# Performance work log

Measured on AMD Instinct MI355X. Metric: run time of the kernel, lower is better.

## Reference

```python
import jax, jax.numpy as jnp
import numpy as np

B, S, D, H, M, E, K = 4, 2048, 1024, 2048, 64, 8, 2  # batch, seq, d_model, max_neurons, moe_hidden, experts, top_k


def setup_inputs() -> dict:
    key = jax.random.key(0)
    ks = jax.random.split(key, 10)
    r = lambda k, shape: jax.random.normal(k, shape, dtype=jnp.float32) * 0.02
    return {
        "inputs_embeds": jax.random.normal(ks[0], (B, S, D), dtype=jnp.float32),
        "enc_W": r(ks[1], (D, H)), "enc_b": jnp.zeros((H,), jnp.float32),
        "s2c_W": r(ks[2], (H, M)), "s2c_b": jnp.zeros((M,), jnp.float32),
        "rW1": r(ks[3], (M, 64)), "rb1": jnp.zeros((64,), jnp.float32),
        "rW2": r(ks[4], (64, E)), "rb2": jnp.zeros((E,), jnp.float32),
        "We1": r(ks[5], (E, M, H // 2)), "be1": jnp.zeros((E, H // 2), jnp.float32),
        "We2": r(ks[6], (E, H // 2, M)), "be2": jnp.zeros((E, M), jnp.float32),
        "c2s_W": r(ks[7], (M, H)), "c2s_b": jnp.zeros((H,), jnp.float32),
        "dec_W": r(ks[8], (H, D)), "dec_b": jnp.zeros((D,), jnp.float32),
        "ln_g": jnp.ones((D,), jnp.float32), "ln_b": jnp.zeros((D,), jnp.float32),
    }


def _layernorm(x, g, b, eps=1e-5):
    mu = x.mean(-1, keepdims=True)
    var = ((x - mu) ** 2).mean(-1, keepdims=True)
    return (x - mu) * jax.lax.rsqrt(var + eps) * g + b


def _forward(inputs_embeds, enc_W, enc_b, s2c_W, s2c_b, rW1, rb1, rW2, rb2,
             We1, be1, We2, be2, c2s_W, c2s_b, dec_W, dec_b, ln_g, ln_b):
    b, s, _ = inputs_embeds.shape
    # GIFNeuron encoder (rate-coded surrogate spikes)
    spikes_enc = jax.nn.sigmoid(inputs_embeds @ enc_W + enc_b)          # (B,S,H)
    flat = spikes_enc.reshape(b * s, H)                                  # (N,H)
    # SpikeToContinuousBridge ('rate'): projection to MoE hidden
    cont = flat @ s2c_W + s2c_b                                          # (N,M)
    # LiquidMoERouter: 2-layer router, softmax, top-k, renormalize
    logits = jnp.tanh(cont @ rW1 + rb1) @ rW2 + rb2                      # (N,E)
    probs = jax.nn.softmax(logits, axis=-1)
    topw, topi = jax.lax.top_k(probs, K)                                 # (N,K)
    w = topw / topw.sum(-1, keepdims=True)
    # dense per-token per-expert gate == sum_k weights[:,k] * (indices[:,k]==e)
    gates = (jax.nn.one_hot(topi, E, dtype=cont.dtype) * w[..., None]).sum(1)  # (N,E)
    # SNNExpert MLP per expert, dense dispatch + weighted combine (index_add equivalent)
    h = jax.nn.relu(jnp.einsum('nm,emh->enh', cont, We1) + be1[:, None, :])    # (E,N,H/2)
    expert_out = jnp.einsum('enh,ehm->enm', h, We2) + be2[:, None, :]          # (E,N,M)
    output_flat = jnp.einsum('enm,ne->nm', expert_out, gates)                  # (N,M)
    # ContinuousToSpikeBridge ('poisson', expected rate), 2D -> 1 timestep
    spikes_moe = jax.nn.sigmoid(output_flat @ c2s_W + c2s_b).reshape(b, s, H)
    # GIFNeuron decoder + LayerNorm
    decoded = jax.nn.sigmoid(spikes_moe @ dec_W + dec_b)                 # (B,S,D)
    return _layernorm(decoded, ln_g, ln_b)


def reference(inputs_embeds, enc_W, enc_b, s2c_W, s2c_b, rW1, rb1, rW2, rb2,
              We1, be1, We2, be2, c2s_W, c2s_b, dec_W, dec_b, ln_g, ln_b):
    return _forward(inputs_embeds, enc_W, enc_b, s2c_W, s2c_b, rW1, rb1, rW2, rb2,
                    We1, be1, We2, be2, c2s_W, c2s_b, dec_W, dec_b, ln_g, ln_b)
```

## Files before the change

kernel.cpp:

```cpp
#include <hip/hip_runtime.h>
#include <hip/hip_bf16.h>
#include <cstdint>
#include <cstddef>

#define TOK    8192
#define DMODEL 1024
#define HDIM   2048
#define MDIM   64
#define NEXP   8
#define HHALF  1024

using f32x4  = __attribute__((ext_vector_type(4))) float;
using bf16x8 = __attribute__((ext_vector_type(8))) __bf16;
using bf16x4 = __attribute__((ext_vector_type(4))) __bf16;

__device__ __forceinline__ void async16(const void* g, void* l) {
  __builtin_amdgcn_global_load_lds(
      (const __attribute__((address_space(1))) unsigned int*)g,
      (__attribute__((address_space(3))) unsigned int*)l, 16, 0, 0);
}

__global__ __launch_bounds__(256) void preamble_kernel(
    const float* __restrict__ X, __bf16* __restrict__ Xb,
    const float* __restrict__ encW, __bf16* __restrict__ encWT,
    const float* __restrict__ s2cW, __bf16* __restrict__ s2cWT,
    const float* __restrict__ c2sW, __bf16* __restrict__ c2sWT,
    const float* __restrict__ decW, __bf16* __restrict__ decWT,
    const float* __restrict__ We1, __bf16* __restrict__ We1T,
    const float* __restrict__ We2, __bf16* __restrict__ We2T) {
  __shared__ float ts[32][33];
  const int tid = threadIdx.x;
  int b = blockIdx.x;
  if (b < 8192) {
    int i = b * 256 + tid;
    float4 v = ((const float4*)X)[i];
    bf16x4 o = { (__bf16)v.x, (__bf16)v.y, (__bf16)v.z, (__bf16)v.w };
    ((bf16x4*)Xb)[i] = o;
    return;
  }
  b -= 8192;
  const float* in; __bf16* outp; int R, C, tx, ty;
  if (b < 2048)              { in = encW; outp = encWT; R = 1024; C = 2048; tx = b % 64; ty = b / 64; }
  else if ((b -= 2048) < 128){ in = s2cW; outp = s2cWT; R = 2048; C = 64;   tx = b % 2;  ty = b / 2;  }
  else if ((b -= 128) < 128) { in = c2sW; outp = c2sWT; R = 64;   C = 2048; tx = b % 64; ty = b / 64; }
  else if ((b -= 128) < 2048){ in = decW; outp = decWT; R = 2048; C = 1024; tx = b % 32; ty = b / 32; }
  else if ((b -= 2048) < 512){ int s = b / 64, t = b % 64;
                               in = We1 + (size_t)s * 65536; outp = We1T + (size_t)s * 65536;
                               R = 64; C = 1024; tx = t % 32; ty = t / 32; }
  else                       { b -= 512; int s = b / 64, t = b % 64;
                               in = We2 + (size_t)s * 65536; outp = We2T + (size_t)s * 65536;
                               R = 1024; C = 64; tx = t % 2; ty = t / 2; }
  const int c0 = tx * 32, r0 = ty * 32;
  const int x = tid & 31, y = tid >> 5;
  #pragma unroll
  for (int i = y; i < 32; i += 8) ts[i][x] = in[(size_t)(r0 + i) * C + c0 + x];
  __syncthreads();
  #pragma unroll
  for (int i = y; i < 32; i += 8)
    outp[(size_t)(c0 + i) * R + r0 + x] = (__bf16)ts[x][i];
}
#define PREAMBLE_BLOCKS (8192 + 2048 + 128 + 128 + 2048 + 512 + 512)

template <int BN, int OUT_BF16, int ACT, int BIAS>
__global__ __launch_bounds__(512, 2) void gemm_8p(
    const __bf16* __restrict__ A, const __bf16* __restrict__ Bt,
    const float* __restrict__ bias, void* __restrict__ Cout,
    int M, int N, int K) {
  constexpr int BM = 256, BK = 64;
  constexpr int WTN = BN / 64;
  constexpr int A_LOADS = 4;
  constexpr int B_LOADS = BN / 64;
  __shared__ __bf16 As[2 * BM * BK];
  __shared__ __bf16 Bs[2 * BN * BK];
  const int tid = threadIdx.x;
  const int wave = tid >> 6, lane = tid & 63;
  const int quad = lane >> 4, l16 = lane & 15;
  const int m0 = blockIdx.x * BM, n0 = blockIdx.y * BN;
  const int wm = (wave & 1) * 128;
  const int wn = (wave >> 1) * (BN / 4);
  const int lrow = lane >> 3, lchunk = lane & 7;
  f32x4 acc[8][WTN] = {};

  const __bf16* aSrc[A_LOADS];
  const __bf16* bSrc[B_LOADS];
  #pragma unroll
  for (int t = 0; t < A_LOADS; ++t) {
    int row = (t * 8 + wave) * 8 + lrow;
    aSrc[t] = A + (size_t)(m0 + row) * K + (lchunk ^ (row & 7)) * 8;
  }
  #pragma unroll
  for (int t = 0; t < B_LOADS; ++t) {
    int row = (t * 8 + wave) * 8 + lrow;
    bSrc[t] = Bt + (size_t)(n0 + row) * K + (lchunk ^ (row & 7)) * 8;
  }
  int aOff[8], bOff[WTN];
  #pragma unroll
  for (int rf = 0; rf < 8; ++rf) {
    int row = wm + rf * 16 + l16;
    aOff[rf] = row * BK + ((quad ^ (row & 7)) * 8);
  }
  #pragma unroll
  for (int cf = 0; cf < WTN; ++cf) {
    int row = wn + cf * 16 + l16;
    bOff[cf] = row * BK + ((quad ^ (row & 7)) * 8);
  }

  auto stageA = [&](int t, __bf16* Ad) {
    async16(aSrc[t], Ad + (t * 8 + wave) * 8 * BK);
    aSrc[t] += BK;
  };
  auto stageB = [&](int t, __bf16* Bd) {
    async16(bSrc[t], Bd + (t * 8 + wave) * 8 * BK);
    bSrc[t] += BK;
  };

  __bf16 *curA = As, *nxtA = As + BM * BK;
  __bf16 *curB = Bs, *nxtB = Bs + BN * BK;
  const int nt = K / BK;

  stageB(0, curB); stageB(1, curB);
  if constexpr (BN == 256) { stageB(2, curB); stageB(3, curB); }
  stageA(0, curA); stageA(2, curA);
  stageA(1, curA); stageA(3, curA);
  asm volatile("s_waitcnt vmcnt(0)" ::: "memory");
  __builtin_amdgcn_s_barrier();

  for (int t = 0; t < nt; ++t) {
    const bool pre = (t + 1 < nt);
    bf16x8 af[4], bv[WTN];
    #pragma unroll
    for (int r = 0; r < 4; ++r) af[r] = *(const bf16x8*)(curA + aOff[r]);
    #pragma unroll
    for (int c = 0; c < WTN; ++c) bv[c] = *(const bf16x8*)(curB + bOff[c]);
    if (pre) {
      stageB(0, nxtB); stageB(1, nxtB);
      asm volatile("s_waitcnt vmcnt(2)" ::: "memory");
    } else {
      asm volatile("s_waitcnt vmcnt(0)" ::: "memory");
    }
    __builtin_amdgcn_s_barrier();
    __builtin_amdgcn_sched_barrier(0);
    __builtin_amdgcn_s_setprio(1);
    #pragma unroll
    for (int c = 0; c < WTN; ++c)
      #pragma unroll
      for (int r = 0; r < 4; ++r)
        acc[r][c] = __builtin_amdgcn_mfma_f32_16x16x32_bf16(af[r], bv[c], acc[r][c], 0, 0, 0);
    __builtin_amdgcn_s_setprio(0);
    __builtin_amdgcn_s_barrier();
    bf16x8 ag[4];
    #pragma unroll
    for (int r = 0; r < 4; ++r) ag[r] = *(const bf16x8*)(curA + aOff[4 + r]);
    if (pre) {
      if constexpr (BN == 256) { stageB(2, nxtB); stageB(3, nxtB); }
      else                     { stageA(0, nxtA); stageA(2, nxtA); }
    }
    __builtin_amdgcn_s_barrier();
    __builtin_amdgcn_sched_barrier(0);
    __builtin_amdgcn_s_setprio(1);
    #pragma unroll
    for (int c = 0; c < WTN; ++c)
      #pragma unroll
      for (int r = 0; r < 4; ++r)
        acc[4 + r][c] = __builtin_amdgcn_mfma_f32_16x16x32_bf16(ag[r], bv[c], acc[4 + r][c], 0, 0, 0);
    __builtin_amdgcn_s_setprio(0);
    __builtin_amdgcn_s_barrier();
    bf16x8 af2[4], bw[WTN];
    #pragma unroll
    for (int r = 0; r < 4; ++r) af2[r] = *(const bf16x8*)(curA + (aOff[r] ^ 32));
    #pragma unroll
    for (int c = 0; c < WTN; ++c) bw[c] = *(const bf16x8*)(curB + (bOff[c] ^ 32));
    if (pre) {
      if constexpr (BN == 256) { stageA(0, nxtA); stageA(2, nxtA); }
      else {
        stageA(1, nxtA); stageA(3, nxtA);
        asm volatile("s_waitcnt vmcnt(2)" ::: "memory");
      }
    }
    __builtin_amdgcn_s_barrier();
    __builtin_amdgcn_sched_barrier(0);
    __builtin_amdgcn_s_setprio(1);
    #pragma unroll
    for (int c = 0; c < WTN; ++c)
      #pragma unroll
      for (int r = 0; r < 4; ++r)
        acc[r][c] = __builtin_amdgcn_mfma_f32_16x16x32_bf16(af2[r], bw[c], acc[r][c], 0, 0, 0);
    __builtin_amdgcn_s_setprio(0);
    __builtin_amdgcn_s_barrier();
    bf16x8 ag2[4];
    #pragma unroll
    for (int r = 0; r < 4; ++r) ag2[r] = *(const bf16x8*)(curA + (aOff[4 + r] ^ 32));
    if (pre) {
      if constexpr (BN == 256) {
        stageA(1, nxtA); stageA(3, nxtA);
        asm volatile("s_waitcnt vmcnt(2)" ::: "memory");
      }
    }
    __builtin_amdgcn_s_barrier();
    __builtin_amdgcn_sched_barrier(0);
    __builtin_amdgcn_s_setprio(1);
    #pragma unroll
    for (int c = 0; c < WTN; ++c)
      #pragma unroll
      for (int r = 0; r < 4; ++r)
        acc[4 + r][c] = __builtin_amdgcn_mfma_f32_16x16x32_bf16(ag2[r], bw[c], acc[4 + r][c], 0, 0, 0);
    __builtin_amdgcn_s_setprio(0);
    __builtin_amdgcn_s_barrier();

    __bf16* x;
    x = curA; curA = nxtA; nxtA = x;
    x = curB; curB = nxtB; nxtB = x;
  }

  #pragma unroll
  for (int rf = 0; rf < 8; ++rf)
    #pragma unroll
    for (int cf = 0; cf < WTN; ++cf)
      #pragma unroll
      for (int r = 0; r < 4; ++r) {
        int m = m0 + wm + rf * 16 + quad * 4 + r;
        int n = n0 + wn + cf * 16 + l16;
        float v = acc[rf][cf][r];
        if (BIAS) v += bias[n];
        if (ACT == 1) v = 1.0f / (1.0f + __expf(-v));
        if (OUT_BF16)
          ((__bf16*)Cout)[(size_t)m * N + n] = (__bf16)v;
        else
          ((float*)Cout)[(size_t)m * N + n] = v;
      }
}

template <int BM, int BN, int WAVES, int OUT_BF16, int ACT, int BIAS, int SUMA>
__global__ __launch_bounds__(WAVES * 64) void gemm_bt(
    const __bf16* __restrict__ A, const __bf16* __restrict__ Bt,
    const float* __restrict__ bias, void* __restrict__ Cout,
    int M, int N, int K, const __bf16* __restrict__ A2) {
  constexpr int BK = 64;
  constexpr int WAVES_N = WAVES / 2;
  constexpr int WTM = BM / 32;
  constexpr int WTN = BN / (WAVES_N * 16);
  constexpr int NBUF = SUMA ? 1 : 2;
  constexpr int A_ISSUES = BM / (8 * WAVES);
  constexpr int B_ISSUES = BN / (8 * WAVES);
  __shared__ __bf16 As[NBUF * BM * BK];
  __shared__ __bf16 Bs[NBUF * BN * BK];
  const int tid = threadIdx.x;
  const int wave = tid >> 6, lane = tid & 63;
  const int quad = lane >> 4, l16 = lane & 15;
  const int m0 = blockIdx.x * BM, n0 = blockIdx.y * BN;
  const int ks = K / gridDim.z;
  const int kbeg = blockIdx.z * ks;
  const int wm = (wave & 1) * (BM / 2);
  const int wn = (wave >> 1) * (BN / WAVES_N);
  const int lrow = lane >> 3;
  const int lchunk = lane & 7;
  f32x4 acc[WTM][WTN] = {};

  const __bf16* aSrc[A_ISSUES];
  const __bf16* bSrc[B_ISSUES];
  #pragma unroll
  for (int t = 0; t < A_ISSUES; ++t) {
    int row = (t * WAVES + wave) * 8 + lrow;
    aSrc[t] = A + (size_t)(m0 + row) * K + kbeg + (lchunk ^ (row & 7)) * 8;
  }
  #pragma unroll
  for (int t = 0; t < B_ISSUES; ++t) {
    int row = (t * WAVES + wave) * 8 + lrow;
    bSrc[t] = Bt + (size_t)(n0 + row) * K + kbeg + (lchunk ^ (row & 7)) * 8;
  }
  int aOff[WTM][2], bOff[WTN][2];
  #pragma unroll
  for (int i = 0; i < WTM; ++i) {
    int row = wm + i * 16 + l16;
    #pragma unroll
    for (int kk = 0; kk < 2; ++kk)
      aOff[i][kk] = row * BK + (((kk * 4 + quad) ^ (row & 7)) * 8);
  }
  #pragma unroll
  for (int j = 0; j < WTN; ++j) {
    int row = wn + j * 16 + l16;
    #pragma unroll
    for (int kk = 0; kk < 2; ++kk)
      bOff[j][kk] = row * BK + (((kk * 4 + quad) ^ (row & 7)) * 8);
  }

  auto stage = [&](__bf16* Ad, __bf16* Bd) {
    #pragma unroll
    for (int t = 0; t < A_ISSUES; ++t) {
      async16(aSrc[t], Ad + (t * WAVES + wave) * 8 * BK);
      aSrc[t] += BK;
    }
    #pragma unroll
    for (int t = 0; t < B_ISSUES; ++t) {
      async16(bSrc[t], Bd + (t * WAVES + wave) * 8 * BK);
      bSrc[t] += BK;
    }
  };
  auto compute = [&](const __bf16* Ab, const __bf16* Bb) {
    #pragma unroll
    for (int kk = 0; kk < 2; ++kk) {
      bf16x8 af[WTM], bfr[WTN];
      #pragma unroll
      for (int i = 0; i < WTM; ++i) af[i] = *(const bf16x8*)(Ab + aOff[i][kk]);
      #pragma unroll
      for (int j = 0; j < WTN; ++j) bfr[j] = *(const bf16x8*)(Bb + bOff[j][kk]);
      #pragma unroll
      for (int i = 0; i < WTM; ++i)
        #pragma unroll
        for (int j = 0; j < WTN; ++j)
          acc[i][j] = __builtin_amdgcn_mfma_f32_16x16x32_bf16(af[i], bfr[j], acc[i][j], 0, 0, 0);
    }
  };

  const int niter = ks / BK;
  if constexpr (SUMA) {
    for (int it = 0; it < niter; ++it) {
      __syncthreads();
      #pragma unroll
      for (int t = 0; t < A_ISSUES; ++t) {
        int row = (t * WAVES + wave) * 8 + lrow;
        size_t go = (size_t)(m0 + row) * K + kbeg + it * BK + lchunk * 8;
        bf16x8 a0 = *(const bf16x8*)(A + go);
        bf16x8 a1 = *(const bf16x8*)(A2 + go);
        bf16x8 s;
        #pragma unroll
        for (int q = 0; q < 8; ++q) s[q] = (__bf16)((float)a0[q] + (float)a1[q]);
        *(bf16x8*)(As + row * BK + ((lchunk ^ (row & 7)) * 8)) = s;
      }
      #pragma unroll
      for (int t = 0; t < B_ISSUES; ++t) {
        async16(bSrc[t], Bs + (t * WAVES + wave) * 8 * BK);
        bSrc[t] += BK;
      }
      __syncthreads();
      compute(As, Bs);
    }
  } else {
    __bf16* curA = As;  __bf16* nxtA = As + BM * BK;
    __bf16* curB = Bs;  __bf16* nxtB = Bs + BN * BK;
    stage(curA, curB);
    asm volatile("s_waitcnt vmcnt(0)" ::: "memory");
    __builtin_amdgcn_s_barrier();
    for (int it = 0; it < niter - 1; ++it) {
      stage(nxtA, nxtB);
      compute(curA, curB);
      asm volatile("s_waitcnt vmcnt(0)" ::: "memory");
      __builtin_amdgcn_s_barrier();
      { __bf16* t = curA; curA = nxtA; nxtA = t; }
      { __bf16* t = curB; curB = nxtB; nxtB = t; }
    }
    compute(curA, curB);
  }

  char* Cz = (char*)Cout + (size_t)blockIdx.z * M * N * (OUT_BF16 ? 2 : 4);
  #pragma unroll
  for (int i = 0; i < WTM; ++i)
    #pragma unroll
    for (int j = 0; j < WTN; ++j)
      #pragma unroll
      for (int r = 0; r < 4; ++r) {
        int m = m0 + wm + i * 16 + quad * 4 + r;
        int n = n0 + wn + j * 16 + l16;
        float v = acc[i][j][r];
        if (BIAS) v += bias[n];
        if (ACT == 1) v = 1.0f / (1.0f + __expf(-v));
        if (OUT_BF16)
          ((__bf16*)Cz)[(size_t)m * N + n] = (__bf16)v;
        else
          ((float*)Cz)[(size_t)m * N + n] = v;
      }
}

__global__ __launch_bounds__(256) void router_kernel(
    const float* __restrict__ contP, const float* __restrict__ s2c_b,
    const float* __restrict__ rW1, const float* __restrict__ rb1,
    const float* __restrict__ rW2, const float* __restrict__ rb2,
    __bf16* __restrict__ contB, int* __restrict__ e01,
    float2* __restrict__ g01, int* __restrict__ cnt) {
  if (blockIdx.x == 0 && threadIdx.x < NEXP) cnt[threadIdx.x] = 0;
  const int wave = threadIdx.x >> 6, lane = threadIdx.x & 63;
  const int n = blockIdx.x * 4 + wave;
  const size_t base = (size_t)n * 64 + lane;
  const size_t slab = (size_t)TOK * 64;
  float c = contP[base] + contP[base + slab] + contP[base + 2 * slab] +
            contP[base + 3 * slab] + s2c_b[lane];
  contB[base] = (__bf16)c;
  float acc = rb1[lane];
  #pragma unroll
  for (int i = 0; i < 64; ++i) {
    float ci = __shfl(c, i);
    acc = fmaf(ci, rW1[i * 64 + lane], acc);
  }
  float t = tanhf(acc);
  float logit[8];
  #pragma unroll
  for (int e = 0; e < 8; ++e) {
    float v = t * rW2[lane * 8 + e];
    #pragma unroll
    for (int o = 32; o; o >>= 1) v += __shfl_xor(v, o);
    logit[e] = v + rb2[e];
  }
  float mx = logit[0];
  #pragma unroll
  for (int e = 1; e < 8; ++e) mx = fmaxf(mx, logit[e]);
  float p[8];
  #pragma unroll
  for (int e = 0; e < 8; ++e) p[e] = __expf(logit[e] - mx);
  float v0 = p[0]; int e0 = 0;
  #pragma unroll
  for (int e = 1; e < 8; ++e) if (p[e] > v0) { v0 = p[e]; e0 = e; }
  float v1 = -1.0f; int e1 = 0;
  #pragma unroll
  for (int e = 0; e < 8; ++e) if (e != e0 && p[e] > v1) { v1 = p[e]; e1 = e; }
  float inv = 1.0f / (v0 + v1);
  if (lane == 0) {
    e01[n] = e0 | (e1 << 8);
    g01[n] = make_float2(v0 * inv, v1 * inv);
  }
}

__global__ __launch_bounds__(256) void fill_kernel(
    const int* __restrict__ e01, int* __restrict__ cnt,
    unsigned* __restrict__ idxb) {
  __shared__ int lcnt[NEXP], lbase[NEXP];
  const int tid = threadIdx.x;
  if (tid < NEXP) lcnt[tid] = 0;
  __syncthreads();
  const int n = blockIdx.x * 256 + tid;
  const int pe = e01[n];
  const int e0 = pe & 0xff, e1 = (pe >> 8) & 0xff;
  const int p0 = atomicAdd(&lcnt[e0], 1);
  const int p1 = atomicAdd(&lcnt[e1], 1);
  __syncthreads();
  if (tid < NEXP) lbase[tid] = atomicAdd(&cnt[tid], lcnt[tid]);
  __syncthreads();
  idxb[e0 * TOK + lbase[e0] + p0] = (unsigned)n;
  idxb[e1 * TOK + lbase[e1] + p1] = (unsigned)n | 0x80000000u;
}

__global__ __launch_bounds__(256) void moe_sparse_kernel(
    const __bf16* __restrict__ contB, const __bf16* __restrict__ We1T,
    const __bf16* __restrict__ We2T, const float* __restrict__ be1,
    const float* __restrict__ be2, const unsigned* __restrict__ idxb,
    const int* __restrict__ cnt, const float2* __restrict__ g01,
    __bf16* __restrict__ slab0, __bf16* __restrict__ slab1) {
  constexpr int TT = 64;
  const int e = blockIdx.y;
  const int start = blockIdx.x * TT;
  const int ne = cnt[e];
  if (start >= ne) return;
  const int nval = min(TT, ne - start);
  __shared__ __bf16 cont_s[TT * 64];
  __shared__ __bf16 w1_s[64 * 64];
  __shared__ __bf16 w2_s[64 * 64];
  __shared__ __bf16 h_s[TT * 64];
  __shared__ unsigned tok_s[TT];
  __shared__ float gate_s[TT];
  const int tid = threadIdx.x;
  const int wave = tid >> 6, lane = tid & 63;
  const int quad = lane >> 4, l16 = lane & 15;
  if (tid < TT) {
    unsigned v = idxb[e * TOK + start + ((tid < nval) ? tid : 0)];
    unsigned tok = v & 0x7fffffffu;
    float2 g = g01[tok];
    tok_s[tid] = v;
    gate_s[tid] = (v >> 31) ? g.y : g.x;
  }
  __syncthreads();
  for (int i = tid; i < TT * 8; i += 256) {
    int r = i >> 3, cc = i & 7;
    unsigned tok = tok_s[r] & 0x7fffffffu;
    *(uint4*)(cont_s + r * 64 + ((cc ^ (r & 7)) * 8)) =
        *(const uint4*)(contB + (size_t)tok * 64 + cc * 8);
  }
  const int wtok = wave * 16;
  f32x4 acc2[4] = {};
  for (int hc = 0; hc < HHALF; hc += 64) {
    __syncthreads();
    for (int c = tid; c < 512; c += 256) {
      int r = c >> 3, cc = c & 7;
      *(uint4*)(w1_s + r * 64 + ((cc ^ (r & 7)) * 8)) =
          *(const uint4*)(We1T + ((size_t)e * HHALF + hc + r) * 64 + cc * 8);
      *(uint4*)(w2_s + r * 64 + ((cc ^ (r & 7)) * 8)) =
          *(const uint4*)(We2T + ((size_t)e * 64 + r) * HHALF + hc + cc * 8);
    }
    __syncthreads();
    f32x4 acc1[4] = {};
    #pragma unroll
    for (int kk = 0; kk < 2; ++kk) {
      bf16x8 af, bfr[4];
      {
        int row = wtok + l16;
        af = *(const bf16x8*)(cont_s + row * 64 + (((kk * 4 + quad) ^ (row & 7)) * 8));
      }
      #pragma unroll
      for (int j = 0; j < 4; ++j) {
        int row = j * 16 + l16;
        bfr[j] = *(const bf16x8*)(w1_s + row * 64 + (((kk * 4 + quad) ^ (row & 7)) * 8));
      }
      #pragma unroll
      for (int j = 0; j < 4; ++j)
        acc1[j] = __builtin_amdgcn_mfma_f32_16x16x32_bf16(af, bfr[j], acc1[j], 0, 0, 0);
    }
    #pragma unroll
    for (int j = 0; j < 4; ++j)
      #pragma unroll
      for (int r = 0; r < 4; ++r) {
        int tr = wtok + quad * 4 + r;
        int hcol = j * 16 + l16;
        float v = acc1[j][r] + be1[e * HHALF + hc + hcol];
        h_s[tr * 64 + (((hcol >> 3) ^ (tr & 7)) * 8) + (hcol & 7)] =
            (__bf16)fmaxf(v, 0.0f);
      }
    #pragma unroll
    for (int kk = 0; kk < 2; ++kk) {
      bf16x8 af, bfr[4];
      {
        int row = wtok + l16;
        af = *(const bf16x8*)(h_s + row * 64 + (((kk * 4 + quad) ^ (row & 7)) * 8));
      }
      #pragma unroll
      for (int j = 0; j < 4; ++j) {
        int row = j * 16 + l16;
        bfr[j] = *(const bf16x8*)(w2_s + row * 64 + (((kk * 4 + quad) ^ (row & 7)) * 8));
      }
      #pragma unroll
      for (int j = 0; j < 4; ++j)
        acc2[j] = __builtin_amdgcn_mfma_f32_16x16x32_bf16(af, bfr[j], acc2[j], 0, 0, 0);
    }
  }
  #pragma unroll
  for (int j = 0; j < 4; ++j)
    #pragma unroll
    for (int r = 0; r < 4; ++r) {
      int tr = wtok + quad * 4 + r;
      if (tr < nval) {
        unsigned v = tok_s[tr];
        unsigned tok = v & 0x7fffffffu;
        int m = j * 16 + l16;
        float o = gate_s[tr] * (acc2[j][r] + be2[e * 64 + m]);
        __bf16* slab = (v >> 31) ? slab1 : slab0;
        slab[(size_t)tok * 64 + m] = (__bf16)o;
      }
    }
}

__global__ __launch_bounds__(256) void ln_kernel(
    const float* __restrict__ x, const float* __restrict__ g,
    const float* __restrict__ b, float* __restrict__ out) {
  const int row = blockIdx.x;
  const float4 v = ((const float4*)(x + (size_t)row * 1024))[threadIdx.x];
  float s1 = v.x + v.y + v.z + v.w;
  float s2 = v.x * v.x + v.y * v.y + v.z * v.z + v.w * v.w;
  #pragma unroll
  for (int o = 32; o; o >>= 1) { s1 += __shfl_xor(s1, o); s2 += __shfl_xor(s2, o); }
  __shared__ float ws1[4], ws2[4];
  const int wave = threadIdx.x >> 6, lane = threadIdx.x & 63;
  if (lane == 0) { ws1[wave] = s1; ws2[wave] = s2; }
  __syncthreads();
  s1 = ws1[0] + ws1[1] + ws1[2] + ws1[3];
  s2 = ws2[0] + ws2[1] + ws2[2] + ws2[3];
  const float mu = s1 * (1.0f / 1024.0f);
  const float var = s2 * (1.0f / 1024.0f) - mu * mu;
  const float inv = rsqrtf(var + 1e-5f);
  const int col = threadIdx.x * 4;
  const float4 gv = *(const float4*)(g + col);
  const float4 bv = *(const float4*)(b + col);
  float4 o;
  o.x = (v.x - mu) * inv * gv.x + bv.x;
  o.y = (v.y - mu) * inv * gv.y + bv.y;
  o.z = (v.z - mu) * inv * gv.z + bv.z;
  o.w = (v.w - mu) * inv * gv.w + bv.w;
  *(float4*)(out + (size_t)row * 1024 + col) = o;
}

extern "C" void kernel_launch(void* const* d_in, const int* in_sizes, int n_in,
                              void* d_out, int out_size, void* d_ws, size_t ws_size,
                              hipStream_t stream) {
  const float* X     = (const float*)d_in[0];
  const float* enc_W = (const float*)d_in[1];
  const float* enc_b = (const float*)d_in[2];
  const float* s2c_W = (const float*)d_in[3];
  const float* s2c_b = (const float*)d_in[4];
  const float* rW1   = (const float*)d_in[5];
  const float* rb1   = (const float*)d_in[6];
  const float* rW2   = (const float*)d_in[7];
  const float* rb2   = (const float*)d_in[8];
  const float* We1   = (const float*)d_in[9];
  const float* be1   = (const float*)d_in[10];
  const float* We2   = (const float*)d_in[11];
  const float* be2   = (const float*)d_in[12];
  const float* c2s_W = (const float*)d_in[13];
  const float* c2s_b = (const float*)d_in[14];
  const float* dec_W = (const float*)d_in[15];
  const float* dec_b = (const float*)d_in[16];
  const float* ln_g  = (const float*)d_in[17];
  const float* ln_b  = (const float*)d_in[18];
  float* out = (float*)d_out;

  char* ws = (char*)d_ws;
  size_t off = 0;
  auto take = [&](size_t bytes) -> char* {
    char* p = ws + off;
    off = (off + bytes + 255) & ~(size_t)255;
    return p;
  };
  const size_t SLAB = (size_t)TOK * HDIM * 2;
  char*   slabA     = take(SLAB);
  char*   slabB     = take(SLAB);
  __bf16* encWT     = (__bf16*)take((size_t)HDIM * DMODEL * 2);
  __bf16* s2cWT     = (__bf16*)take((size_t)MDIM * HDIM * 2);
  __bf16* c2sWT     = (__bf16*)take((size_t)HDIM * MDIM * 2);
  __bf16* decWT     = (__bf16*)take((size_t)DMODEL * HDIM * 2);
  __bf16* We1T      = (__bf16*)take((size_t)NEXP * HHALF * MDIM * 2);
  __bf16* We2T      = (__bf16*)take((size_t)NEXP * MDIM * HHALF * 2);
  __bf16* contB     = (__bf16*)take((size_t)TOK * MDIM * 2);
  int*    e01       = (int*)take((size_t)TOK * 4);
  float2* g01       = (float2*)take((size_t)TOK * 8);
  __bf16* oslab0    = (__bf16*)take((size_t)TOK * MDIM * 2);
  __bf16* oslab1    = (__bf16*)take((size_t)TOK * MDIM * 2);
  int*     cnt      = (int*)take((size_t)NEXP * 4);
  unsigned* idxb    = (unsigned*)take((size_t)NEXP * TOK * 4);
  if (off > ws_size) return;

  __bf16* Xb        = (__bf16*)slabA;
  float*  contP     = (float*)(slabA + (size_t)TOK * DMODEL * 2);
  __bf16* spikesMoe = (__bf16*)slabA;
  __bf16* spikesEnc = (__bf16*)slabB;
  float*  decoded   = (float*)slabB;

  preamble_kernel<<<PREAMBLE_BLOCKS, 256, 0, stream>>>(
      X, Xb, enc_W, encWT, s2c_W, s2cWT, c2s_W, c2sWT, dec_W, decWT,
      We1, We1T, We2, We2T);

  gemm_8p<256, 1, 1, 1><<<dim3(TOK / 256, HDIM / 256), 512, 0, stream>>>(
      Xb, encWT, enc_b, spikesEnc, TOK, HDIM, DMODEL);
  gemm_bt<128, 64, 4, 0, 0, 0, 0><<<dim3(TOK / 128, 1, 4), 256, 0, stream>>>(
      spikesEnc, s2cWT, nullptr, contP, TOK, MDIM, HDIM, nullptr);
  router_kernel<<<TOK / 4, 256, 0, stream>>>(contP, s2c_b, rW1, rb1, rW2, rb2,
                                             contB, e01, g01, cnt);
  fill_kernel<<<TOK / 256, 256, 0, stream>>>(e01, cnt, idxb);
  moe_sparse_kernel<<<dim3(TOK / 64, NEXP), 256, 0, stream>>>(
      contB, We1T, We2T, be1, be2, idxb, cnt, g01, oslab0, oslab1);
  gemm_bt<128, 128, 4, 1, 1, 1, 1><<<dim3(TOK / 128, HDIM / 128, 1), 256, 0, stream>>>(
      oslab0, c2sWT, c2s_b, spikesMoe, TOK, HDIM, MDIM, oslab1);
  gemm_8p<128, 0, 1, 1><<<dim3(TOK / 256, DMODEL / 128), 512, 0, stream>>>(
      spikesMoe, decWT, dec_b, decoded, TOK, DMODEL, HDIM);
  ln_kernel<<<TOK, 256, 0, stream>>>(decoded, ln_g, ln_b, out);
}
```

Baseline: 304.7 us.

## Double-buffer MoE expert weights with async LDS loads and reorder GEMM prefetch

Result: no change. 300.4 us (-1.4%).

```diff
diff --git a/kernel.cpp b/kernel.cpp
--- a/kernel.cpp
+++ b/kernel.cpp
@@ -118,9 +118,9 @@
   __bf16 *curB = Bs, *nxtB = Bs + BN * BK;
   const int nt = K / BK;
 
+  stageA(0, curA); stageA(2, curA);
   stageB(0, curB); stageB(1, curB);
   if constexpr (BN == 256) { stageB(2, curB); stageB(3, curB); }
-  stageA(0, curA); stageA(2, curA);
   stageA(1, curA); stageA(3, curA);
   asm volatile("s_waitcnt vmcnt(0)" ::: "memory");
   __builtin_amdgcn_s_barrier();
@@ -133,68 +133,61 @@
     #pragma unroll
     for (int c = 0; c < WTN; ++c) bv[c] = *(const bf16x8*)(curB + bOff[c]);
     if (pre) {
+      stageA(0, nxtA); stageA(2, nxtA);
       stageB(0, nxtB); stageB(1, nxtB);
+      asm volatile("s_waitcnt vmcnt(4)" ::: "memory");
+    } else {
+      asm volatile("s_waitcnt vmcnt(0)" ::: "memory");
+    }
+    __builtin_amdgcn_s_barrier();
+    __builtin_amdgcn_sched_barrier(0);
+    __builtin_amdgcn_s_setprio(1);
+    #pragma unroll
+    for (int c = 0; c < WTN; ++c)
+      #pragma unroll
+      for (int r = 0; r < 4; ++r)
+        acc[r][c] = __builtin_amdgcn_mfma_f32_16x16x32_bf16(af[r], bv[c], acc[r][c], 0, 0, 0);
+    __builtin_amdgcn_s_setprio(0);
+    __builtin_amdgcn_s_barrier();
+    bf16x8 ag[4];
+    #pragma unroll
+    for (int r = 0; r < 4; ++r) ag[r] = *(const bf16x8*)(curA + aOff[4 + r]);
+    if (pre) {
+      if constexpr (BN == 256) { stageB(2, nxtB); stageB(3, nxtB); }
+    }
+    __builtin_amdgcn_s_barrier();
+    __builtin_amdgcn_sched_barrier(0);
+    __builtin_amdgcn_s_setprio(1);
+    #pragma unroll
+    for (int c = 0; c < WTN; ++c)
+      #pragma unroll
+      for (int r = 0; r < 4; ++r)
+        acc[4 + r][c] = __builtin_amdgcn_mfma_f32_16x16x32_bf16(ag[r], bv[c], acc[4 + r][c], 0, 0, 0);
+    __builtin_amdgcn_s_setprio(0);
+    __builtin_amdgcn_s_barrier();
+    bf16x8 af2[4], bw[WTN];
+    #pragma unroll
+    for (int r = 0; r < 4; ++r) af2[r] = *(const bf16x8*)(curA + (aOff[r] ^ 32));
+    #pragma unroll
+    for (int c = 0; c < WTN; ++c) bw[c] = *(const bf16x8*)(curB + (bOff[c] ^ 32));
+    if (pre) { stageA(1, nxtA); stageA(3, nxtA); }
+    __builtin_amdgcn_s_barrier();
+    __builtin_amdgcn_sched_barrier(0);
+    __builtin_amdgcn_s_setprio(1);
+    #pragma unroll
+    for (int c = 0; c < WTN; ++c)
+      #pragma unroll
+      for (int r = 0; r < 4; ++r)
+        acc[r][c] = __builtin_amdgcn_mfma_f32_16x16x32_bf16(af2[r], bw[c], acc[r][c], 0, 0, 0);
+    __builtin_amdgcn_s_setprio(0);
+    __builtin_amdgcn_s_barrier();
+    bf16x8 ag2[4];
+    #pragma unroll
+    for (int r = 0; r < 4; ++r) ag2[r] = *(const bf16x8*)(curA + (aOff[4 + r] ^ 32));
+    if (pre) {
       asm volatile("s_waitcnt vmcnt(2)" ::: "memory");
     } else {
       asm volatile("s_waitcnt vmcnt(0)" ::: "memory");
-    }
-    __builtin_amdgcn_s_barrier();
-    __builtin_amdgcn_sched_barrier(0);
-    __builtin_amdgcn_s_setprio(1);
-    #pragma unroll
-    for (int c = 0; c < WTN; ++c)
-      #pragma unroll
-      for (int r = 0; r < 4; ++r)
-        acc[r][c] = __builtin_amdgcn_mfma_f32_16x16x32_bf16(af[r], bv[c], acc[r][c], 0, 0, 0);
-    __builtin_amdgcn_s_setprio(0);
-    __builtin_amdgcn_s_barrier();
-    bf16x8 ag[4];
-    #pragma unroll
-    for (int r = 0; r < 4; ++r) ag[r] = *(const bf16x8*)(curA + aOff[4 + r]);
-    if (pre) {
-      if constexpr (BN == 256) { stageB(2, nxtB); stageB(3, nxtB); }
-      else                     { stageA(0, nxtA); stageA(2, nxtA); }
-    }
-    __builtin_amdgcn_s_barrier();
-    __builtin_amdgcn_sched_barrier(0);
-    __builtin_amdgcn_s_setprio(1);
-    #pragma unroll
-    for (int c = 0; c < WTN; ++c)
-      #pragma unroll
-      for (int r = 0; r < 4; ++r)
-        acc[4 + r][c] = __builtin_amdgcn_mfma_f32_16x16x32_bf16(ag[r], bv[c], acc[4 + r][c], 0, 0, 0);
-    __builtin_amdgcn_s_setprio(0);
-    __builtin_amdgcn_s_barrier();
-    bf16x8 af2[4], bw[WTN];
-    #pragma unroll
-    for (int r = 0; r < 4; ++r) af2[r] = *(const bf16x8*)(curA + (aOff[r] ^ 32));
-    #pragma unroll
-    for (int c = 0; c < WTN; ++c) bw[c] = *(const bf16x8*)(curB + (bOff[c] ^ 32));
-    if (pre) {
-      if constexpr (BN == 256) { stageA(0, nxtA); stageA(2, nxtA); }
-      else {
-        stageA(1, nxtA); stageA(3, nxtA);
-        asm volatile("s_waitcnt vmcnt(2)" ::: "memory");
-      }
-    }
-    __builtin_amdgcn_s_barrier();
-    __builtin_amdgcn_sched_barrier(0);
-    __builtin_amdgcn_s_setprio(1);
-    #pragma unroll
-    for (int c = 0; c < WTN; ++c)
-      #pragma unroll
-      for (int r = 0; r < 4; ++r)
-        acc[r][c] = __builtin_amdgcn_mfma_f32_16x16x32_bf16(af2[r], bw[c], acc[r][c], 0, 0, 0);
-    __builtin_amdgcn_s_setprio(0);
-    __builtin_amdgcn_s_barrier();
-    bf16x8 ag2[4];
-    #pragma unroll
-    for (int r = 0; r < 4; ++r) ag2[r] = *(const bf16x8*)(curA + (aOff[4 + r] ^ 32));
-    if (pre) {
-      if constexpr (BN == 256) {
-        stageA(1, nxtA); stageA(3, nxtA);
-        asm volatile("s_waitcnt vmcnt(2)" ::: "memory");
-      }
     }
     __builtin_amdgcn_s_barrier();
     __builtin_amdgcn_sched_barrier(0);
@@ -451,8 +444,8 @@
   if (start >= ne) return;
   const int nval = min(TT, ne - start);
   __shared__ __bf16 cont_s[TT * 64];
-  __shared__ __bf16 w1_s[64 * 64];
-  __shared__ __bf16 w2_s[64 * 64];
+  __shared__ __bf16 w1_s[2][64 * 64];
+  __shared__ __bf16 w2_s[2][64 * 64];
   __shared__ __bf16 h_s[TT * 64];
   __shared__ unsigned tok_s[TT];
   __shared__ float gate_s[TT];
@@ -473,18 +466,29 @@
     *(uint4*)(cont_s + r * 64 + ((cc ^ (r & 7)) * 8)) =
         *(const uint4*)(contB + (size_t)tok * 64 + cc * 8);
   }
+  auto stageW = [&](int hc, int buf) {
+    #pragma unroll
+    for (int b = 0; b < 2; ++b) {
+      int c = b * 256 + wave * 64 + lane;
+      int r = c >> 3, s = c & 7;
+      async16(We1T + ((size_t)e * HHALF + hc + r) * 64 + ((s ^ (r & 7)) * 8),
+              w1_s[buf] + (b * 256 + wave * 64) * 8);
+      async16(We2T + ((size_t)e * 64 + r) * HHALF + hc + ((s ^ (r & 7)) * 8),
+              w2_s[buf] + (b * 256 + wave * 64) * 8);
+    }
+  };
+  stageW(0, 0);
+  asm volatile("s_waitcnt vmcnt(0)" ::: "memory");
+  __syncthreads();
+
   const int wtok = wave * 16;
   f32x4 acc2[4] = {};
-  for (int hc = 0; hc < HHALF; hc += 64) {
-    __syncthreads();
-    for (int c = tid; c < 512; c += 256) {
-      int r = c >> 3, cc = c & 7;
-      *(uint4*)(w1_s + r * 64 + ((cc ^ (r & 7)) * 8)) =
-          *(const uint4*)(We1T + ((size_t)e * HHALF + hc + r) * 64 + cc * 8);
-      *(uint4*)(w2_s + r * 64 + ((cc ^ (r & 7)) * 8)) =
-          *(const uint4*)(We2T + ((size_t)e * 64 + r) * HHALF + hc + cc * 8);
-    }
-    __syncthreads();
+  int cur = 0;
+  for (int i = 0; i < HHALF / 64; ++i) {
+    const int hc = i * 64;
+    if (i + 1 < HHALF / 64) stageW(hc + 64, cur ^ 1);
+    const __bf16* w1c = w1_s[cur];
+    const __bf16* w2c = w2_s[cur];
     f32x4 acc1[4] = {};
     #pragma unroll
     for (int kk = 0; kk < 2; ++kk) {
@@ -496,7 +500,7 @@
       #pragma unroll
       for (int j = 0; j < 4; ++j) {
         int row = j * 16 + l16;
-        bfr[j] = *(const bf16x8*)(w1_s + row * 64 + (((kk * 4 + quad) ^ (row & 7)) * 8));
+        bfr[j] = *(const bf16x8*)(w1c + row * 64 + (((kk * 4 + quad) ^ (row & 7)) * 8));
       }
       #pragma unroll
       for (int j = 0; j < 4; ++j)
@@ -522,11 +526,16 @@
       #pragma unroll
       for (int j = 0; j < 4; ++j) {
         int row = j * 16 + l16;
-        bfr[j] = *(const bf16x8*)(w2_s + row * 64 + (((kk * 4 + quad) ^ (row & 7)) * 8));
+        bfr[j] = *(const bf16x8*)(w2c + row * 64 + (((kk * 4 + quad) ^ (row & 7)) * 8));
       }
       #pragma unroll
       for (int j = 0; j < 4; ++j)
         acc2[j] = __builtin_amdgcn_mfma_f32_16x16x32_bf16(af, bfr[j], acc2[j], 0, 0, 0);
+    }
+    if (i + 1 < HHALF / 64) {
+      asm volatile("s_waitcnt vmcnt(0)" ::: "memory");
+      __syncthreads();
+      cur ^= 1;
     }
   }
   #pragma unroll
```
